# Kernel tuning notes

Measured on AMD Instinct MI355X. Metric: run time of the kernel, lower is better.

## Reference

```python
import jax, jax.numpy as jnp
import numpy as np

N_NODES = 100000
N_EDGES = 1600000
N_GRAPHS = 512
N_REL = 4
N_TYPES = 13
EMB = 128
HID = 128
BN_EPS = 1e-5
L2_EPS = 1e-12


def setup_inputs() -> dict:
    key = jax.random.key(0)
    ks = jax.random.split(key, 16)
    node_type = jax.random.randint(ks[0], (N_NODES,), 0, N_TYPES)
    x = jax.nn.one_hot(node_type, N_TYPES, dtype=jnp.float32)  # [N,13] one-hot
    edge_index = jax.random.randint(ks[1], (2, N_EDGES), 0, N_NODES)
    edge_type = jax.random.randint(ks[2], (N_EDGES,), 0, N_REL)
    batch = jnp.sort(jax.random.randint(ks[3], (N_NODES,), 0, N_GRAPHS))
    s = 0.05
    return {
        "x": x,
        "edge_index": edge_index,
        "edge_type": edge_type,
        "batch": batch,
        "emb": jax.random.normal(ks[4], (N_TYPES, EMB), jnp.float32) * s,
        "Wrel": jax.random.normal(ks[5], (2, N_REL, HID, HID), jnp.float32) * s,  # layer0 in=EMB==HID
        "Wroot": jax.random.normal(ks[6], (2, HID, HID), jnp.float32) * s,
        "conv_bias": jnp.zeros((2, HID), jnp.float32),
        "bn_gamma": jnp.ones((2, HID), jnp.float32),
        "bn_beta": jnp.zeros((2, HID), jnp.float32),
        "prelu_a": jnp.full((2,), 0.25, jnp.float32),
        "fc1_w": jax.random.normal(ks[7], (HID, 256), jnp.float32) * s,
        "fc1_b": jnp.zeros((256,), jnp.float32),
        "fc2_w": jax.random.normal(ks[8], (256, 128), jnp.float32) * s,
        "fc2_b": jnp.zeros((128,), jnp.float32),
        "out_w": jax.random.normal(ks[9], (128, 1), jnp.float32) * s,
        "out_b": jnp.zeros((1,), jnp.float32),
    }


def _rgcn_conv(h, Wrel, Wroot, bias, src, dst, edge_type):
    # PyG RGCNConv: out = h @ Wroot + bias + sum_r mean_{edges of rel r}(h_src @ W_r)
    n = h.shape[0]
    out = h @ Wroot + bias
    for r in range(N_REL):
        m = (edge_type == r).astype(h.dtype)  # [E]
        hr = h @ Wrel[r]                       # [N, dout]
        msg = hr[src] * m[:, None]             # gather + mask  [E, dout]
        num = jax.ops.segment_sum(msg, dst, num_segments=n)
        cnt = jax.ops.segment_sum(m, dst, num_segments=n)
        out = out + num / jnp.maximum(cnt, 1.0)[:, None]
    return out


def _batchnorm(h, gamma, beta):
    mu = jnp.mean(h, axis=0)
    var = jnp.mean((h - mu) ** 2, axis=0)  # biased var (training-mode BN)
    return (h - mu) * jax.lax.rsqrt(var + BN_EPS) * gamma + beta


def reference(x, edge_index, edge_type, batch, emb, Wrel, Wroot, conv_bias,
              bn_gamma, bn_beta, prelu_a, fc1_w, fc1_b, fc2_w, fc2_b, out_w, out_b):
    src, dst = edge_index[0], edge_index[1]
    idx = jnp.argmax(x, axis=1)         # torch.nonzero(one_hot)[1]
    h = emb[idx]                        # [N, EMB]
    for l in range(2):
        h = _rgcn_conv(h, Wrel[l], Wroot[l], conv_bias[l], src, dst, edge_type)
        h = _batchnorm(h, bn_gamma[l], bn_beta[l])
        h = jnp.where(h >= 0, h, prelu_a[l] * h)  # PReLU
        nrm = jnp.sqrt(jnp.sum(h * h, axis=1, keepdims=True))
        h = h / jnp.maximum(nrm, L2_EPS)          # F.normalize(p=2, dim=1)
    # global mean pool over graphs
    pooled = jax.ops.segment_sum(h, batch, num_segments=N_GRAPHS)
    cnt = jax.ops.segment_sum(jnp.ones((h.shape[0],), h.dtype), batch, num_segments=N_GRAPHS)
    g = pooled / jnp.maximum(cnt, 1.0)[:, None]   # [G, HID]
    g = jax.nn.relu(g @ fc1_w + fc1_b)
    g = jax.nn.relu(g @ fc2_w + fc2_b)
    return g @ out_w + out_b                      # [G, 1]
```

## Files before the change

### kernel.cpp

```cpp
#include <hip/hip_runtime.h>
#include <hip/hip_bf16.h>

#define NN 100000
#define NE 1600000
#define NG 512
#define CH3 65536
#define CHW 16384
#define NCH 2
#define BPC 128
#define ES 12500


typedef __attribute__((ext_vector_type(8))) short short8;
typedef __attribute__((ext_vector_type(4))) float float4v;


__device__ inline int lower_bound_dev(const int* __restrict__ a, int n, int v) {
    int lo = 0, hi = n;
    while (lo < hi) { int mid = (lo + hi) >> 1; if (a[mid] < v) lo = mid + 1; else hi = mid; }
    return lo;
}

__device__ inline unsigned short f2bf(float x) {
    unsigned u = __float_as_uint(x);
    unsigned r = (u + 0x7fffu + ((u >> 16) & 1u)) >> 16;
    return (unsigned short)r;
}


__global__ void node_type_kernel(const float* __restrict__ x, int* __restrict__ idx, int n) {
    int i = blockIdx.x * blockDim.x + threadIdx.x;
    if (i >= n) return;
    const float* row = x + (size_t)i * 13;
    int b = 0;
    #pragma unroll
    for (int t = 0; t < 13; ++t) if (row[t] > 0.5f) { b = t; }
    idx[i] = b;
}


__global__ void build_weights(const float* __restrict__ emb, const float* __restrict__ Wroot,
                              const float* __restrict__ Wrel,
                              unsigned short* __restrict__ Bf, unsigned short* __restrict__ B0f,
                              float* __restrict__ bnSums, float* __restrict__ bnSums1,
                              float* __restrict__ g0) {
    if (blockIdx.x < 8) bnSums[blockIdx.x * 256 + threadIdx.x] = 0.f;
    else if (blockIdx.x < 16) bnSums1[(blockIdx.x - 8) * 256 + threadIdx.x] = 0.f;
    int i = blockIdx.x * 256 + threadIdx.x;
    if (i < 81920) {
        int j = i & 7;
        int lane = (i >> 3) & 63;
        int t = (i >> 9) & 7;
        int ks = (i >> 12) & 3;
        int kc = i >> 14;
        int n = t * 16 + (lane & 15);
        int kcol = j * 16 + ks * 4 + (lane >> 4);
        float w;
        if (kc == 0) w = Wroot[16384 + (size_t)kcol * 128 + n];
        else {
            int r = kc - 1;
            w = Wrel[(((size_t)(4 + r) * 128) + kcol) * 128 + n];
        }
        Bf[i] = f2bf(w);
    } else if (i < 94208) {
        int i0 = i - 81920;
        int j = i0 & 7;
        int lane = (i0 >> 3) & 63;
        int t = (i0 >> 9) & 7;
        int ks = i0 >> 12;
        int n = t * 16 + (lane & 15);
        int p = ks * 32 + (lane >> 4) * 8 + j;
        float val = 0.f;
        if (p < 32) {
            if (p < 13) {
                const float* er = emb + (size_t)p * 128;
                const float* wc = Wroot + n;
                float acc = 0.f;
                for (int k = 0; k < 128; ++k) acc += er[k] * wc[(size_t)k * 128];
                val = acc;
            }
        } else {
            int r = (p - 32) >> 4, tt = (p - 32) & 15;
            if (tt < 13) {
                const float* er = emb + (size_t)tt * 128;
                const float* wc = Wrel + ((size_t)r * 128) * 128 + n;
                float acc = 0.f;
                for (int k = 0; k < 128; ++k) acc += er[k] * wc[(size_t)k * 128];
                val = acc;
            }
        }
        B0f[i0] = f2bf(val);
    } else {
        int gz = i - 94208;
        g0[gz] = 0.f;
    }
}


__global__ __launch_bounds__(256) void hist_kernel(const int* __restrict__ dst,
                                                   const int* __restrict__ src,
                                                   const int* __restrict__ et,
                                                   const int* __restrict__ ntype,
                                                   int* __restrict__ srcT,
                                                   unsigned* __restrict__ partials) {
    __shared__ unsigned h[CHW];
    const int b = blockIdx.x, c = blockIdx.y;
    const int lo = c * CH3;
    for (int i = threadIdx.x; i < CHW; i += 256) h[i] = 0;
    __syncthreads();
    const int e0 = b * ES;
    const int e1 = (e0 + ES < NE) ? e0 + ES : NE;
    if (c == 0) {
        for (int e = e0 + threadIdx.x; e < e1; e += 256) {
            int k = dst[e] - lo;
            if (k >= 0 && k < CH3) atomicAdd(&h[k >> 2], 1u << ((k & 3) << 3));
            int s = src[e];
            srcT[e] = s | (ntype[s] << 17) | (et[e] << 21);
        }
    } else {
        for (int e = e0 + threadIdx.x; e < e1; e += 256) {
            int k = dst[e] - lo;
            if (k >= 0 && k < CH3) atomicAdd(&h[k >> 2], 1u << ((k & 3) << 3));
        }
    }
    __syncthreads();
    unsigned* out = partials + ((size_t)(c * BPC + b)) * CHW;
    for (int i = threadIdx.x; i < CHW; i += 256) out[i] = h[i];
}

__global__ __launch_bounds__(256) void hr_scan1(unsigned* __restrict__ partials,
                                                int* __restrict__ offs,
                                                int* __restrict__ bsums, int n) {
    __shared__ int wsum[4];
    const int b = blockIdx.x;
    const int tid = threadIdx.x;
    const int c = b >> 6;
    const int i = (b & 63) * 256 + tid;
    size_t base = (size_t)c * BPC * CHW + i;
    unsigned r0 = 0, r1 = 0, r2 = 0, r3 = 0;
    #pragma unroll 4
    for (int bb = 0; bb < BPC; ++bb) {
        unsigned t = partials[base + (size_t)bb * CHW];
        partials[base + (size_t)bb * CHW] = r0 | (r1 << 8) | (r2 << 16) | (r3 << 24);
        r0 += t & 0xffu; r1 += (t >> 8) & 0xffu; r2 += (t >> 16) & 0xffu; r3 += t >> 24;
    }
    int v[4] = {(int)r0, (int)r1, (int)r2, (int)r3};
    int loc = v[0] + v[1] + v[2] + v[3];
    const int lane = tid & 63, wid = tid >> 6;
    int sc = loc;
    #pragma unroll
    for (int o = 1; o < 64; o <<= 1) { int t = __shfl_up(sc, o, 64); if (lane >= o) sc += t; }
    if (lane == 63) wsum[wid] = sc;
    __syncthreads();
    int wbase = 0;
    for (int w = 0; w < wid; ++w) wbase += wsum[w];
    int run = wbase + sc - loc;
    const int key0 = b * 1024 + tid * 4;
    #pragma unroll
    for (int j = 0; j < 4; ++j) { int idx = key0 + j; if (idx < n) offs[idx] = run; run += v[j]; }
    if (tid == 255) bsums[b] = wbase + sc;
}

__global__ __launch_bounds__(256) void scan23(int* __restrict__ offs, const int* __restrict__ bsums,
                                              int nb, int n) {
    __shared__ int part[256];
    const int tid = threadIdx.x;
    int v = (tid < nb && tid < blockIdx.x) ? bsums[tid] : 0;
    part[tid] = v;
    __syncthreads();
    #pragma unroll
    for (int o = 128; o > 0; o >>= 1) {
        if (tid < o) part[tid] += part[tid + o];
        __syncthreads();
    }
    const int s = part[0];
    const int base = blockIdx.x * 1024 + tid * 4;
    #pragma unroll
    for (int j = 0; j < 4; ++j) { int idx = base + j; if (idx < n) offs[idx] += s; }
    if (blockIdx.x == (unsigned)(nb - 1) && tid == 0) offs[n] = s + bsums[nb - 1];
}

__global__ __launch_bounds__(256) void place_kernel(const int* __restrict__ dst,
                                                    const int* __restrict__ srcT,
                                                    const int* __restrict__ offs,
                                                    const unsigned* __restrict__ partials,
                                                    int* __restrict__ sortedSrc) {
    __shared__ unsigned cur[CHW];
    const int b = blockIdx.x, c = blockIdx.y;
    const int lo = c * CH3;
    const unsigned* pb = partials + ((size_t)(c * BPC + b)) * CHW;
    for (int i = threadIdx.x; i < CHW; i += 256) cur[i] = pb[i];
    __syncthreads();
    const int e0 = b * ES;
    const int e1 = (e0 + ES < NE) ? e0 + ES : NE;
    for (int e = e0 + threadIdx.x; e < e1; e += 256) {
        int key = dst[e];
        int k = key - lo;
        if (k >= 0 && k < CH3) {
            int sh = (k & 3) << 3;
            unsigned old = atomicAdd(&cur[k >> 2], 1u << sh);
            int my = (int)((old >> sh) & 0xffu);
            int pos = offs[key] + my;
            sortedSrc[pos] = srcT[e];
        }
    }
}


__global__ __launch_bounds__(256) void gemm0_fused(const int* __restrict__ sortedSrc,
                                                   const int* __restrict__ offs,
                                                   const int* __restrict__ ntype,
                                                   const unsigned short* __restrict__ B0f,
                                                   const float* __restrict__ bias,
                                                   unsigned short* __restrict__ Cb,
                                                   float* __restrict__ bnSums, int M) {
    __shared__ unsigned short A0L[12 * 128 * 8];
    __shared__ unsigned cnt[256][13];
    __shared__ float sred[2][4][128];
    const int tid = threadIdx.x;

    {
        const int node = tid & 127;
        const int half = tid >> 7;
        const int n = blockIdx.x * 128 + node;
        #pragma unroll
        for (int t = 0; t < 13; ++t) cnt[tid][t] = 0;
        if (n < M) {
            const int o0 = offs[n], o1 = offs[n + 1];
            const int mid = (o0 + o1) >> 1;
            const int lo = half ? mid : o0;
            const int hi = half ? o1 : mid;
            for (int i = lo; i < hi; ++i) {
                int v = sortedSrc[i];
                int ty = (v >> 17) & 15, r = v >> 21;
                cnt[tid][ty] += 1u << (r << 3);
            }
        }
    }
    __syncthreads();

    if (tid < 128) {
        const int n = blockIdx.x * 128 + tid;
        const int tile = tid >> 4, l16 = tid & 15;
        if (n < M) {
            unsigned cw[13]; unsigned relc = 0;
            #pragma unroll
            for (int t = 0; t < 13; ++t) { cw[t] = cnt[tid][t] + cnt[tid + 128][t]; relc += cw[t]; }
            float inv[4];
            #pragma unroll
            for (int r = 0; r < 4; ++r) {
                unsigned c = (relc >> (r << 3)) & 0xffu;
                inv[r] = 1.0f / (float)(c > 0 ? c : 1);
            }
            const int myty = ntype[n];
            #pragma unroll
            for (int ks = 0; ks < 3; ++ks) {
                #pragma unroll
                for (int quad = 0; quad < 4; ++quad) {
                    unsigned short vals[8];
                    #pragma unroll
                    for (int j = 0; j < 8; ++j) {
                        int p = ks * 32 + quad * 8 + j;
                        float v;
                        if (p < 32) v = (p == myty) ? 1.0f : 0.0f;
                        else {
                            int r = (p - 32) >> 4, tt = (p - 32) & 15;
                            v = (tt < 13) ? (float)((cw[tt] >> (r << 3)) & 0xffu) * inv[r] : 0.0f;
                        }
                        vals[j] = f2bf(v);
                    }
                    const int C = ks * 4 + quad;
                    *(uint4*)(A0L + (C * 128 + tile * 16 + l16) * 8) = *(uint4*)vals;
                }
            }
        } else {
            uint4 z; z.x = 0; z.y = 0; z.z = 0; z.w = 0;
            #pragma unroll
            for (int C = 0; C < 12; ++C)
                *(uint4*)(A0L + (C * 128 + tile * 16 + l16) * 8) = z;
        }
    }
    __syncthreads();

    const int wv = tid >> 6, lane = tid & 63;
    const int l16 = lane & 15, quad = lane >> 4;
    const int rowbase = blockIdx.x * 128 + wv * 32;
    const int tileL0 = wv * 2, tileL1 = wv * 2 + 1;

    float4v acc[2][8];
    #pragma unroll
    for (int t = 0; t < 8; ++t) {
        float bv = bias[t * 16 + l16];
        float4v av = {bv, bv, bv, bv};
        acc[0][t] = av; acc[1][t] = av;
    }

    const unsigned short* bl = B0f + lane * 8;
    #pragma unroll
    for (int ks = 0; ks < 3; ++ks) {
        const int C = ks * 4 + quad;
        short8 af0 = *(const short8*)(A0L + (C * 128 + tileL0 * 16 + l16) * 8);
        short8 af1 = *(const short8*)(A0L + (C * 128 + tileL1 * 16 + l16) * 8);
        const unsigned short* bp = bl + ((ks * 8) << 9);
        #pragma unroll
        for (int t = 0; t < 8; ++t) {
            short8 bf = *(const short8*)(bp + (t << 9));
            acc[0][t] = __builtin_amdgcn_mfma_f32_16x16x32_bf16(af0, bf, acc[0][t], 0, 0, 0);
            acc[1][t] = __builtin_amdgcn_mfma_f32_16x16x32_bf16(af1, bf, acc[1][t], 0, 0, 0);
        }
    }

    #pragma unroll
    for (int h = 0; h < 2; ++h) {
        #pragma unroll
        for (int rg = 0; rg < 4; ++rg) {
            int rr = rowbase + h * 16 + quad * 4 + rg;
            if (rr < M) {
                unsigned short v[8];
                #pragma unroll
                for (int t = 0; t < 8; ++t) v[t] = f2bf(acc[h][t][rg]);
                *(uint4*)(Cb + (size_t)rr * 128 + l16 * 8) = *(uint4*)v;
            }
        }
    }
    float s[8], q[8];
    #pragma unroll
    for (int t = 0; t < 8; ++t) {
        s[t] = 0.f; q[t] = 0.f;
        #pragma unroll
        for (int h = 0; h < 2; ++h) {
            #pragma unroll
            for (int rg = 0; rg < 4; ++rg) {
                int rr = rowbase + h * 16 + quad * 4 + rg;
                if (rr < M) { float v = acc[h][t][rg]; s[t] += v; q[t] += v * v; }
            }
        }
    }
    #pragma unroll
    for (int t = 0; t < 8; ++t) {
        s[t] += __shfl_down(s[t], 32, 64); q[t] += __shfl_down(q[t], 32, 64);
        s[t] += __shfl_down(s[t], 16, 64); q[t] += __shfl_down(q[t], 16, 64);
    }
    if (lane < 16) {
        #pragma unroll
        for (int t = 0; t < 8; ++t) {
            sred[0][wv][t * 16 + l16] = s[t];
            sred[1][wv][t * 16 + l16] = q[t];
        }
    }
    __syncthreads();
    if (tid < 128) {
        float S = sred[0][0][tid] + sred[0][1][tid] + sred[0][2][tid] + sred[0][3][tid];
        float Q = sred[1][0][tid] + sred[1][1][tid] + sred[1][2][tid] + sred[1][3][tid];
        float* bnS = bnSums + ((blockIdx.x & 7) << 8);
        unsafeAtomicAdd(bnS + tid, S);
        unsafeAtomicAdd(bnS + 128 + tid, Q);
    }
}


__global__ __launch_bounds__(256) void gather_gemm1(const unsigned short* __restrict__ hbf,
                                                    const int* __restrict__ sortedSrc,
                                                    const int* __restrict__ offs,
                                                    const unsigned short* __restrict__ Bf,
                                                    const float* __restrict__ bias,
                                                    unsigned short* __restrict__ Cb,
                                                    float* __restrict__ bnSums) {
    __shared__ unsigned short rootL[2048];
    __shared__ unsigned short aggL[8192];
    const int tid = threadIdx.x;
    const int tile = blockIdx.x;
    {
        const int l16g = tid >> 4;
        const int cidx = tid & 15;
        const int c8 = cidx << 3;
        const int n = tile * 16 + l16g;
        const int pu = cidx * 16 + (l16g ^ cidx);
        uint4 ru = *(const uint4*)(hbf + (size_t)n * 128 + c8);
        *(uint4*)(rootL + pu * 8) = ru;

        const unsigned short* hb = hbf + c8;
        const int o0 = offs[n], o1 = offs[n + 1];

        float a0[8], a1[8], a2[8], a3[8];
        #pragma unroll
        for (int j = 0; j < 8; ++j) { a0[j] = 0.f; a1[j] = 0.f; a2[j] = 0.f; a3[j] = 0.f; }
        float c0 = 0.f, c1 = 0.f, c2 = 0.f, c3 = 0.f;

        auto body = [&](int v, uint4 u) {
            int r = v >> 21;
            float f[8];
            f[0] = __uint_as_float(u.x << 16); f[1] = __uint_as_float(u.x & 0xffff0000u);
            f[2] = __uint_as_float(u.y << 16); f[3] = __uint_as_float(u.y & 0xffff0000u);
            f[4] = __uint_as_float(u.z << 16); f[5] = __uint_as_float(u.z & 0xffff0000u);
            f[6] = __uint_as_float(u.w << 16); f[7] = __uint_as_float(u.w & 0xffff0000u);
            float m0 = (r == 0) ? 1.f : 0.f, m1 = (r == 1) ? 1.f : 0.f;
            float m2 = (r == 2) ? 1.f : 0.f, m3 = (r == 3) ? 1.f : 0.f;
            c0 += m0; c1 += m1; c2 += m2; c3 += m3;
            #pragma unroll
            for (int j = 0; j < 8; ++j) {
                a0[j] = fmaf(m0, f[j], a0[j]);
                a1[j] = fmaf(m1, f[j], a1[j]);
                a2[j] = fmaf(m2, f[j], a2[j]);
                a3[j] = fmaf(m3, f[j], a3[j]);
            }
        };

        int i = o0;
        for (; i + 4 <= o1; i += 4) {
            int v0 = sortedSrc[i], v1 = sortedSrc[i + 1];
            int v2 = sortedSrc[i + 2], v3 = sortedSrc[i + 3];
            uint4 u0 = *(const uint4*)(hb + (size_t)(v0 & 0x1ffff) * 128);
            uint4 u1 = *(const uint4*)(hb + (size_t)(v1 & 0x1ffff) * 128);
            uint4 u2 = *(const uint4*)(hb + (size_t)(v2 & 0x1ffff) * 128);
            uint4 u3 = *(const uint4*)(hb + (size_t)(v3 & 0x1ffff) * 128);
            body(v0, u0); body(v1, u1); body(v2, u2); body(v3, u3);
        }
        if (i + 2 <= o1) {
            int v0 = sortedSrc[i], v1 = sortedSrc[i + 1];
            uint4 u0 = *(const uint4*)(hb + (size_t)(v0 & 0x1ffff) * 128);
            uint4 u1 = *(const uint4*)(hb + (size_t)(v1 & 0x1ffff) * 128);
            body(v0, u0); body(v1, u1);
            i += 2;
        }
        if (i < o1) {
            int v0 = sortedSrc[i];
            uint4 u0 = *(const uint4*)(hb + (size_t)(v0 & 0x1ffff) * 128);
            body(v0, u0);
        }

        const float i0 = 1.f / fmaxf(c0, 1.f), i1 = 1.f / fmaxf(c1, 1.f);
        const float i2 = 1.f / fmaxf(c2, 1.f), i3 = 1.f / fmaxf(c3, 1.f);
        unsigned short* bp = aggL + pu * 8;
        auto pack = [&](float* a, float inv, unsigned short* dp) {
            unsigned short v[8];
            #pragma unroll
            for (int j = 0; j < 8; ++j) v[j] = f2bf(a[j] * inv);
            *(uint4*)dp = *(uint4*)v;
        };
        pack(a0, i0, bp);
        pack(a1, i1, bp + 2048);
        pack(a2, i2, bp + 4096);
        pack(a3, i3, bp + 6144);
    }
    __syncthreads();

    const int wv = tid >> 6, lane = tid & 63;
    const int l16 = lane & 15, quad = lane >> 4;
    const int t0 = wv << 1;
    float4v acc0, acc1;
    {
        float b0v = bias[t0 * 16 + l16];
        float b1v = bias[(t0 + 1) * 16 + l16];
        float4v a0v = {b0v, b0v, b0v, b0v};
        float4v a1v = {b1v, b1v, b1v, b1v};
        acc0 = a0v; acc1 = a1v;
    }
    const unsigned short* bl = Bf + lane * 8;
    #pragma unroll
    for (int kc = 0; kc < 5; ++kc) {
        const unsigned short* Abase = (kc == 0) ? rootL : (aggL + (kc - 1) * 2048);
        #pragma unroll
        for (int ks = 0; ks < 4; ++ks) {
            const int C = ks * 4 + quad;
            const int p = C * 16 + (l16 ^ C);
            short8 af = *(const short8*)(Abase + p * 8);
            const unsigned short* bp = bl + (((kc * 4 + ks) * 8 + t0) << 9);
            short8 b0 = *(const short8*)(bp);
            short8 b1 = *(const short8*)(bp + 512);
            acc0 = __builtin_amdgcn_mfma_f32_16x16x32_bf16(af, b0, acc0, 0, 0, 0);
            acc1 = __builtin_amdgcn_mfma_f32_16x16x32_bf16(af, b1, acc1, 0, 0, 0);
        }
    }
    const int rowbase = tile * 16;
    #pragma unroll
    for (int rg = 0; rg < 4; ++rg) {
        int rr = rowbase + quad * 4 + rg;
        unsigned pk = (unsigned)f2bf(acc0[rg]) | ((unsigned)f2bf(acc1[rg]) << 16);
        *(unsigned*)(Cb + (size_t)rr * 128 + l16 * 8 + t0) = pk;
    }
    float s0 = 0.f, q0 = 0.f, s1 = 0.f, q1 = 0.f;
    #pragma unroll
    for (int rg = 0; rg < 4; ++rg) {
        float v0 = acc0[rg], v1 = acc1[rg];
        s0 += v0; q0 += v0 * v0; s1 += v1; q1 += v1 * v1;
    }
    s0 += __shfl_down(s0, 32, 64); q0 += __shfl_down(q0, 32, 64);
    s1 += __shfl_down(s1, 32, 64); q1 += __shfl_down(q1, 32, 64);
    s0 += __shfl_down(s0, 16, 64); q0 += __shfl_down(q0, 16, 64);
    s1 += __shfl_down(s1, 16, 64); q1 += __shfl_down(q1, 16, 64);
    if (lane < 16) {
        float* bnS = bnSums + ((tile & 7) << 8);
        unsafeAtomicAdd(bnS + t0 * 16 + l16, s0);
        unsafeAtomicAdd(bnS + 128 + t0 * 16 + l16, q0);
        unsafeAtomicAdd(bnS + (t0 + 1) * 16 + l16, s1);
        unsafeAtomicAdd(bnS + 128 + (t0 + 1) * 16 + l16, q1);
    }
}


__global__ __launch_bounds__(256) void bn_apply_kernel(const unsigned short* __restrict__ Cb,
                                unsigned short* __restrict__ hbf,
                                const float* __restrict__ bnSums,
                                const float* __restrict__ gamma, const float* __restrict__ beta,
                                const float* __restrict__ prelu_a, int layer) {
    __shared__ float finS[256];
    const int tid = threadIdx.x;
    if (tid < 128) {
        float s = 0.f, q = 0.f;
        #pragma unroll
        for (int j = 0; j < 8; ++j) { s += bnSums[j * 256 + tid]; q += bnSums[j * 256 + 128 + tid]; }
        const float invn = 1.0f / (float)NN;
        float mu = s * invn;
        float var = q * invn - mu * mu; if (var < 0.f) var = 0.f;
        finS[tid] = mu;
        finS[128 + tid] = rsqrtf(var + 1e-5f);
    }
    __syncthreads();
    const int row = blockIdx.x * 16 + (tid >> 4);
    const int li = tid & 15;
    const int p8 = li << 3;
    const float a = prelu_a[layer];
    uint4 u = *(const uint4*)(Cb + (size_t)row * 128 + p8);
    float v[8];
    v[0] = __uint_as_float(u.x << 16); v[1] = __uint_as_float(u.x & 0xffff0000u);
    v[2] = __uint_as_float(u.y << 16); v[3] = __uint_as_float(u.y & 0xffff0000u);
    v[4] = __uint_as_float(u.z << 16); v[5] = __uint_as_float(u.z & 0xffff0000u);
    v[6] = __uint_as_float(u.w << 16); v[7] = __uint_as_float(u.w & 0xffff0000u);
    float t[8]; float ss = 0.f;
    #pragma unroll
    for (int j = 0; j < 8; ++j) {
        int cc = j * 16 + li;
        float tv = (v[j] - finS[cc]) * finS[128 + cc] * gamma[cc] + beta[cc];
        tv = (tv >= 0.f) ? tv : a * tv;
        t[j] = tv; ss += tv * tv;
    }
    ss += __shfl_xor(ss, 1, 64);
    ss += __shfl_xor(ss, 2, 64);
    ss += __shfl_xor(ss, 4, 64);
    ss += __shfl_xor(ss, 8, 64);
    const float scale = 1.0f / fmaxf(sqrtf(ss), 1e-12f);
    unsigned short o[8];
    #pragma unroll
    for (int j = 0; j < 8; ++j) o[j] = f2bf(t[j] * scale);
    *(uint4*)(hbf + (size_t)row * 128 + p8) = *(uint4*)o;
}


__global__ __launch_bounds__(256) void bn_apply_pool(const unsigned short* __restrict__ Cb,
                                const float* __restrict__ bnSums,
                                const float* __restrict__ gamma, const float* __restrict__ beta,
                                const float* __restrict__ prelu_a,
                                const int* __restrict__ batch,
                                float* __restrict__ g0) {
    __shared__ float P[16][128];
    __shared__ int gids[16];
    __shared__ float finS[256];
    const int tid = threadIdx.x;
    if (tid < 128) {
        float s = 0.f, q = 0.f;
        #pragma unroll
        for (int j = 0; j < 8; ++j) { s += bnSums[j * 256 + tid]; q += bnSums[j * 256 + 128 + tid]; }
        const float invn = 1.0f / (float)NN;
        float mu = s * invn;
        float var = q * invn - mu * mu; if (var < 0.f) var = 0.f;
        finS[tid] = mu;
        finS[128 + tid] = rsqrtf(var + 1e-5f);
    }
    const int r16 = tid >> 4;
    const int li = tid & 15;
    const int row = blockIdx.x * 16 + r16;
    const int p8 = li << 3;
    if (li == 0) gids[r16] = batch[row];
    __syncthreads();
    const float a = prelu_a[1];
    uint4 u = *(const uint4*)(Cb + (size_t)row * 128 + p8);
    float v[8];
    v[0] = __uint_as_float(u.x << 16); v[1] = __uint_as_float(u.x & 0xffff0000u);
    v[2] = __uint_as_float(u.y << 16); v[3] = __uint_as_float(u.y & 0xffff0000u);
    v[4] = __uint_as_float(u.z << 16); v[5] = __uint_as_float(u.z & 0xffff0000u);
    v[6] = __uint_as_float(u.w << 16); v[7] = __uint_as_float(u.w & 0xffff0000u);
    float t[8]; float ss = 0.f;
    #pragma unroll
    for (int j = 0; j < 8; ++j) {
        int cc = j * 16 + li;
        float tv = (v[j] - finS[cc]) * finS[128 + cc] * gamma[cc] + beta[cc];
        tv = (tv >= 0.f) ? tv : a * tv;
        t[j] = tv; ss += tv * tv;
    }
    ss += __shfl_xor(ss, 1, 64);
    ss += __shfl_xor(ss, 2, 64);
    ss += __shfl_xor(ss, 4, 64);
    ss += __shfl_xor(ss, 8, 64);
    const float scale = 1.0f / fmaxf(sqrtf(ss), 1e-12f);
    #pragma unroll
    for (int j = 0; j < 8; ++j) P[r16][p8 + j] = t[j] * scale;
    __syncthreads();
    if (tid < 128) {
        int cur = gids[0];
        float run = 0.f;
        #pragma unroll
        for (int rr = 0; rr < 16; ++rr) {
            int g = gids[rr];
            if (g != cur) {
                unsafeAtomicAdd(&g0[(size_t)cur * 128 + tid], run);
                run = 0.f; cur = g;
            }
            run += P[rr][tid];
        }
        unsafeAtomicAdd(&g0[(size_t)cur * 128 + tid], run);
    }
}


__global__ __launch_bounds__(256) void mlp_kernel(const float* __restrict__ g,
                                                  const float* __restrict__ w1,
                                                  const float* __restrict__ b1,
                                                  const int* __restrict__ batch,
                                                  const float* __restrict__ w2,
                                                  const float* __restrict__ b2,
                                                  const float* __restrict__ outw,
                                                  const float* __restrict__ outb,
                                                  float* __restrict__ out) {
    __shared__ float g1L[256];
    __shared__ int se[2];
    __shared__ float wsum[2];
    const int row = blockIdx.x;
    const int j = threadIdx.x;
    if (j < 2) se[j] = lower_bound_dev(batch, NN, row + j);
    __syncthreads();
    const int c = se[1] - se[0];
    const float invc = 1.0f / (float)(c > 0 ? c : 1);
    float acc = 0.f;
    #pragma unroll 8
    for (int k = 0; k < 128; ++k) {
        int lk = (k & 7) * 16 + (k >> 3);
        acc += g[row * 128 + k] * w1[lk * 256 + j];
    }
    g1L[j] = fmaxf(acc * invc + b1[j], 0.f);
    __syncthreads();
    if (j < 128) {
        float acc2 = b2[j];
        #pragma unroll 8
        for (int k = 0; k < 256; ++k) acc2 += g1L[k] * w2[k * 128 + j];
        float cc = fmaxf(acc2, 0.f) * outw[j];
        cc += __shfl_down(cc, 32, 64);
        cc += __shfl_down(cc, 16, 64);
        cc += __shfl_down(cc, 8, 64);
        cc += __shfl_down(cc, 4, 64);
        cc += __shfl_down(cc, 2, 64);
        cc += __shfl_down(cc, 1, 64);
        if ((j & 63) == 0) wsum[j >> 6] = cc;
    }
    __syncthreads();
    if (j == 0) out[row] = wsum[0] + wsum[1] + outb[0];
}


extern "C" void kernel_launch(void* const* d_in, const int* in_sizes, int n_in,
                              void* d_out, int out_size, void* d_ws, size_t ws_size,
                              hipStream_t stream) {
    const float* x      = (const float*)d_in[0];
    const int*   eidx   = (const int*)d_in[1];
    const int*   etype  = (const int*)d_in[2];
    const int*   batch  = (const int*)d_in[3];
    const float* emb    = (const float*)d_in[4];
    const float* Wrel   = (const float*)d_in[5];
    const float* Wroot  = (const float*)d_in[6];
    const float* cbias  = (const float*)d_in[7];
    const float* gamma  = (const float*)d_in[8];
    const float* beta   = (const float*)d_in[9];
    const float* prelua = (const float*)d_in[10];
    const float* fc1w   = (const float*)d_in[11];
    const float* fc1b   = (const float*)d_in[12];
    const float* fc2w   = (const float*)d_in[13];
    const float* fc2b   = (const float*)d_in[14];
    const float* outw   = (const float*)d_in[15];
    const float* outb   = (const float*)d_in[16];
    float* out = (float*)d_out;

    const int* src = eidx;
    const int* dst = eidx + NE;

    char* p = (char*)d_ws;
    auto alloc = [&](size_t bytes) { char* r = p; p += (bytes + 255) & ~(size_t)255; return r; };
    unsigned short* hbf   = (unsigned short*)alloc((size_t)NN * 128 * 2);
    unsigned short* Cb    = (unsigned short*)alloc((size_t)NN * 128 * 2);
    unsigned* partials = (unsigned*)alloc((size_t)NCH * BPC * CHW * 4);
    int*   sortedSrc = (int*)alloc((size_t)NE * 4);
    int*   srcT      = (int*)alloc((size_t)NE * 4);
    int*   offs      = (int*)alloc((size_t)(NN + 1) * 4);
    int*   bsums     = (int*)alloc(1024);
    int*   ntype     = (int*)alloc((size_t)NN * 4);
    unsigned short* Bf1 = (unsigned short*)alloc((size_t)81920 * 2);
    unsigned short* B0f = (unsigned short*)alloc((size_t)12288 * 2);
    float* bnSums  = (float*)alloc(2048 * 4);
    float* bnSums1 = (float*)alloc(2048 * 4);
    float* g0      = (float*)alloc((size_t)NG * 128 * 4);

    const int NBLK = (NN + 1023) / 1024;

    node_type_kernel<<<(NN + 255) / 256, 256, 0, stream>>>(x, ntype, NN);
    build_weights<<<624, 256, 0, stream>>>(emb, Wroot, Wrel, Bf1, B0f, bnSums, bnSums1, g0);

    hist_kernel<<<dim3(BPC, NCH), 256, 0, stream>>>(dst, src, etype, ntype, srcT, partials);
    hr_scan1<<<NBLK, 256, 0, stream>>>(partials, offs, bsums, NN);
    scan23<<<NBLK, 256, 0, stream>>>(offs, bsums, NBLK, NN);
    place_kernel<<<dim3(BPC, NCH), 256, 0, stream>>>(dst, srcT, offs, partials, sortedSrc);

    gemm0_fused<<<(NN + 127) / 128, 256, 0, stream>>>(sortedSrc, offs, ntype, B0f,
                                                      cbias, Cb, bnSums, NN);
    bn_apply_kernel<<<NN / 16, 256, 0, stream>>>(Cb, hbf, bnSums, gamma, beta, prelua, 0);

    gather_gemm1<<<NN / 16, 256, 0, stream>>>(hbf, sortedSrc, offs, Bf1, cbias + 128, Cb, bnSums1);
    bn_apply_pool<<<NN / 16, 256, 0, stream>>>(Cb, bnSums1, gamma + 128, beta + 128,
                                               prelua, batch, g0);

    mlp_kernel<<<NG, 256, 0, stream>>>(g0, fc1w, fc1b, batch, fc2w, fc2b, outw, outb, out);
}
```

Before: 345.1 us.

## Fuse node-type kernel into weight build and balance gemm0 edge counting

Folds the one-hot node-type extraction into the weight-building kernel as extra blocks, which removes one kernel launch. The place kernel also packs each edge's destination-local node index into the upper bits of sortedSrc. This lets gemm0_fused count edge types with a flat, block-wide loop over its contiguous edge range using shared-memory atomics, instead of two threads per node walking that node's edges. The aim is better load balance and coalesced reads, at the cost of LDS atomic contention. Readers of the relation bits now mask with &3 so the extra packed bits do not leak into the relation index.

```diff
diff --git a/kernel.cpp b/kernel.cpp
--- a/kernel.cpp
+++ b/kernel.cpp
@@ -28,24 +28,25 @@
 }
 
 
-__global__ void node_type_kernel(const float* __restrict__ x, int* __restrict__ idx, int n) {
-    int i = blockIdx.x * blockDim.x + threadIdx.x;
-    if (i >= n) return;
-    const float* row = x + (size_t)i * 13;
-    int b = 0;
-    #pragma unroll
-    for (int t = 0; t < 13; ++t) if (row[t] > 0.5f) { b = t; }
-    idx[i] = b;
-}
-
-
 __global__ void build_weights(const float* __restrict__ emb, const float* __restrict__ Wroot,
-                              const float* __restrict__ Wrel,
+                              const float* __restrict__ Wrel, const float* __restrict__ x,
                               unsigned short* __restrict__ Bf, unsigned short* __restrict__ B0f,
+                              int* __restrict__ ntype,
                               float* __restrict__ bnSums, float* __restrict__ bnSums1,
                               float* __restrict__ g0) {
     if (blockIdx.x < 8) bnSums[blockIdx.x * 256 + threadIdx.x] = 0.f;
     else if (blockIdx.x < 16) bnSums1[(blockIdx.x - 8) * 256 + threadIdx.x] = 0.f;
+    if (blockIdx.x >= 624) {
+        int i = (blockIdx.x - 624) * 256 + threadIdx.x;
+        if (i < NN) {
+            const float* row = x + (size_t)i * 13;
+            int b = 0;
+            #pragma unroll
+            for (int t = 0; t < 13; ++t) if (row[t] > 0.5f) { b = t; }
+            ntype[i] = b;
+        }
+        return;
+    }
     int i = blockIdx.x * 256 + threadIdx.x;
     if (i < 81920) {
         int j = i & 7;
@@ -201,7 +202,7 @@
             unsigned old = atomicAdd(&cur[k >> 2], 1u << sh);
             int my = (int)((old >> sh) & 0xffu);
             int pos = offs[key] + my;
-            sortedSrc[pos] = srcT[e];
+            sortedSrc[pos] = srcT[e] | ((key & 127) << 23);
         }
     }
 }
@@ -215,26 +216,22 @@
                                                    unsigned short* __restrict__ Cb,
                                                    float* __restrict__ bnSums, int M) {
     __shared__ unsigned short A0L[12 * 128 * 8];
-    __shared__ unsigned cnt[256][13];
+    __shared__ unsigned cnt[128][13];
     __shared__ float sred[2][4][128];
     const int tid = threadIdx.x;
 
+    for (int i = tid; i < 1664; i += 256) ((unsigned*)cnt)[i] = 0;
+    __syncthreads();
     {
-        const int node = tid & 127;
-        const int half = tid >> 7;
-        const int n = blockIdx.x * 128 + node;
-        #pragma unroll
-        for (int t = 0; t < 13; ++t) cnt[tid][t] = 0;
-        if (n < M) {
-            const int o0 = offs[n], o1 = offs[n + 1];
-            const int mid = (o0 + o1) >> 1;
-            const int lo = half ? mid : o0;
-            const int hi = half ? o1 : mid;
-            for (int i = lo; i < hi; ++i) {
-                int v = sortedSrc[i];
-                int ty = (v >> 17) & 15, r = v >> 21;
-                cnt[tid][ty] += 1u << (r << 3);
-            }
+        const int nb = blockIdx.x * 128;
+        const int nEnd = (nb + 128 < M) ? nb + 128 : M;
+        const int oB = offs[nb], oE = offs[nEnd];
+        for (int i = oB + tid; i < oE; i += 256) {
+            int v = sortedSrc[i];
+            int nl = (v >> 23) & 127;
+            int ty = (v >> 17) & 15;
+            int r  = (v >> 21) & 3;
+            atomicAdd(&cnt[nl][ty], 1u << (r << 3));
         }
     }
     __syncthreads();
@@ -245,7 +242,7 @@
         if (n < M) {
             unsigned cw[13]; unsigned relc = 0;
             #pragma unroll
-            for (int t = 0; t < 13; ++t) { cw[t] = cnt[tid][t] + cnt[tid + 128][t]; relc += cw[t]; }
+            for (int t = 0; t < 13; ++t) { cw[t] = cnt[tid][t]; relc += cw[t]; }
             float inv[4];
             #pragma unroll
             for (int r = 0; r < 4; ++r) {
@@ -388,7 +385,7 @@
         float c0 = 0.f, c1 = 0.f, c2 = 0.f, c3 = 0.f;
 
         auto body = [&](int v, uint4 u) {
-            int r = v >> 21;
+            int r = (v >> 21) & 3;
             float f[8];
             f[0] = __uint_as_float(u.x << 16); f[1] = __uint_as_float(u.x & 0xffff0000u);
             f[2] = __uint_as_float(u.y << 16); f[3] = __uint_as_float(u.y & 0xffff0000u);
@@ -700,8 +697,9 @@
 
     const int NBLK = (NN + 1023) / 1024;
 
-    node_type_kernel<<<(NN + 255) / 256, 256, 0, stream>>>(x, ntype, NN);
-    build_weights<<<624, 256, 0, stream>>>(emb, Wroot, Wrel, Bf1, B0f, bnSums, bnSums1, g0);
+    build_weights<<<624 + (NN + 255) / 256, 256, 0, stream>>>(emb, Wroot, Wrel, x,
+                                                              Bf1, B0f, ntype,
+                                                              bnSums, bnSums1, g0);
 
     hist_kernel<<<dim3(BPC, NCH), 256, 0, stream>>>(dst, src, etype, ntype, srcT, partials);
     hr_scan1<<<NBLK, 256, 0, stream>>>(partials, offs, bsums, NN);
```

Result: slower. 357.0 us (+3.5%).
